# Kernel optimization log

Hardware: AMD Instinct MI355X
Metric: run time of the kernel (lower is better)

## Reference

```python
import jax, jax.numpy as jnp
import numpy as np

HIDDEN = 2048
GAMMA = 0.96875
SCALE_BASE = 512  # XPOS default from torchscale / Jamie-Stirling/RetNet


def _xpos(x, downscale=False):
    # x: [B, L, d]. Faithful port of XPOS with offset=0.
    B, L, d = x.shape
    half = d // 2
    # per-dim scale vector: (arange(0,d,2) + 0.4d) / (1.4d)
    scale_vec = (jnp.arange(0, d, 2, dtype=jnp.float32) + 0.4 * d) / (1.4 * d)  # [half]
    power = jnp.arange(L, dtype=jnp.float32) / SCALE_BASE                        # [L]
    scale = scale_vec[None, :] ** power[:, None]                                 # [L, half]
    # fixed_pos_embedding over `half` frequency dims
    inv_freq = 1.0 / (10000.0 ** (jnp.arange(half, dtype=jnp.float32) / half))   # [half]
    sinusoid = jnp.arange(L, dtype=jnp.float32)[:, None] * inv_freq[None, :]     # [L, half]
    sin, cos = jnp.sin(sinusoid), jnp.cos(sinusoid)
    if downscale:
        scale = 1.0 / scale
    # duplicate_interleave: [L, half] -> [L, d] with each column repeated twice
    sin_s = jnp.repeat(sin * scale, 2, axis=-1)  # [L, d]
    cos_s = jnp.repeat(cos * scale, 2, axis=-1)  # [L, d]
    # rotate_every_two
    x1 = x[..., 0::2]
    x2 = x[..., 1::2]
    rot = jnp.stack((-x2, x1), axis=-1).reshape(x.shape)
    return x * cos_s[None] + rot * sin_s[None]


def _decay_matrix(L):
    n = jnp.arange(L)[:, None]
    m = jnp.arange(L)[None, :]
    mask = n >= m
    # clamp exponent to avoid overflow where masked (torch sets NaN->0)
    D = jnp.where(mask, GAMMA ** jnp.maximum(n - m, 0).astype(jnp.float32), 0.0)
    return D  # [L, L]


def setup_inputs() -> dict:
    key = jax.random.key(0)
    kx, kq, kk, kv = jax.random.split(key, 4)
    B, S, H = 4, 2048, HIDDEN
    X = jax.random.normal(kx, (B, S, H), dtype=jnp.float32)
    W_Q = jax.random.normal(kq, (H, H), dtype=jnp.float32) / H
    W_K = jax.random.normal(kk, (H, H), dtype=jnp.float32) / H
    W_V = jax.random.normal(kv, (H, H), dtype=jnp.float32) / H
    return {"X": X, "W_Q": W_Q, "W_K": W_K, "W_V": W_V}


def reference(X, W_Q, W_K, W_V):
    B, S, H = X.shape
    Q = _xpos(X @ W_Q)                   # [B, S, H]
    K = _xpos(X @ W_K, downscale=True)   # [B, S, H]
    V = X @ W_V                          # [B, S, H]
    D = _decay_matrix(S)                 # [S, S]
    att = jnp.einsum("bnh,bmh->bnm", Q, K) * D[None]  # [B, S, S]
    return att @ V                       # [B, S, H]
```

## Files before the change

kernel.cpp:

```cpp
#include <hip/hip_runtime.h>
#include <math.h>


typedef __attribute__((ext_vector_type(8))) short short8;
typedef __attribute__((ext_vector_type(4))) float f32x4;
typedef __attribute__((ext_vector_type(4))) unsigned short us4;

#define BM 128
#define BN 128
#define BK 64

static __device__ __forceinline__ unsigned short f2bf(float f) {
    unsigned int u = __float_as_uint(f);
    u += 0x7FFFu + ((u >> 16) & 1u);
    return (unsigned short)(u >> 16);
}

static __device__ __forceinline__ void gload16(const unsigned short* g, unsigned short* l) {
    __builtin_amdgcn_global_load_lds(
        (const __attribute__((address_space(1))) unsigned int*)g,
        (__attribute__((address_space(3))) unsigned int*)l, 16, 0, 0);
}

template <int STAGE>
__global__ __launch_bounds__(256)
void gemm_bt(const unsigned short* __restrict__ A,
             const unsigned short* __restrict__ Bt,
             void* __restrict__ Cv,
             unsigned short* __restrict__ Cq,
             unsigned short* __restrict__ Ck,
             unsigned short* __restrict__ Cvt,
             int lda, int ldb, int Kd,
             long long sA, long long sB, long long sC)
{
    constexpr int S = 2048, H = 2048;
    const int rowBase = blockIdx.y * BM;
    const int colBase = blockIdx.x * BN;

    if (STAGE == 3 && blockIdx.x > blockIdx.y) {
        unsigned short* att = (unsigned short*)Cv + (long long)blockIdx.z * sC;
        int r = threadIdx.x >> 1, c = (threadIdx.x & 1) * 64;
        unsigned short* p = att + (size_t)(rowBase + r) * S + colBase + c;
        uint4 z = make_uint4(0, 0, 0, 0);
#pragma unroll
        for (int q = 0; q < 8; ++q) ((uint4*)p)[q] = z;
        return;
    }

    A  += (long long)blockIdx.z * sA;
    Bt += (long long)blockIdx.z * sB;

    __shared__ unsigned short As[BM * BK];
    __shared__ unsigned short Bs[BN * BK];

    const int tid  = threadIdx.x;
    const int wave = tid >> 6;
    const int lane = tid & 63;
    const int wm = (wave & 1) * 64;
    const int wn = (wave >> 1) * 64;

    f32x4 acc[4][4];
#pragma unroll
    for (int i = 0; i < 4; ++i)
#pragma unroll
        for (int j = 0; j < 4; ++j) acc[i][j] = (f32x4){0.f, 0.f, 0.f, 0.f};

    int kmax = Kd;
    if (STAGE == 4) { int km = colBase + BN; kmax = km < Kd ? km : Kd; }

    const int srow = wave * 32 + (lane >> 3);
    const int schunk = ((lane & 7) ^ ((lane >> 3) & 7)) * 8;
    const unsigned short* ga = A  + (size_t)(rowBase + srow) * lda + schunk;
    const unsigned short* gb = Bt + (size_t)(colBase + srow) * ldb + schunk;
    unsigned short* lA = As + wave * 2048;
    unsigned short* lB = Bs + wave * 2048;

#pragma unroll
    for (int q = 0; q < 4; ++q) {
        gload16(ga + (size_t)q * 8 * lda, lA + q * 512);
        gload16(gb + (size_t)q * 8 * ldb, lB + q * 512);
    }

    const int fr = lane & 15;
    const int qd = lane >> 4;
    const int fsw = fr & 7;

    for (int k0 = 0; k0 < kmax; k0 += BK) {
        __syncthreads();
        short8 af0[4], bf0[4], af1[4], bf1[4];
#pragma unroll
        for (int i = 0; i < 4; ++i) {
            int row = wm + i * 16 + fr;
            af0[i] = *(const short8*)&As[row * 64 + ((qd ^ fsw) * 8)];
            af1[i] = *(const short8*)&As[row * 64 + (((4 + qd) ^ fsw) * 8)];
        }
#pragma unroll
        for (int j = 0; j < 4; ++j) {
            int row = wn + j * 16 + fr;
            bf0[j] = *(const short8*)&Bs[row * 64 + ((qd ^ fsw) * 8)];
            bf1[j] = *(const short8*)&Bs[row * 64 + (((4 + qd) ^ fsw) * 8)];
        }
        __syncthreads();
        if (k0 + BK < kmax) {
            const unsigned short* ga2 = ga + k0 + BK;
            const unsigned short* gb2 = gb + k0 + BK;
#pragma unroll
            for (int q = 0; q < 4; ++q) {
                gload16(ga2 + (size_t)q * 8 * lda, lA + q * 512);
                gload16(gb2 + (size_t)q * 8 * ldb, lB + q * 512);
            }
        }
#pragma unroll
        for (int i = 0; i < 4; ++i)
#pragma unroll
            for (int j = 0; j < 4; ++j)
                acc[i][j] = __builtin_amdgcn_mfma_f32_16x16x32_bf16(af0[i], bf0[j], acc[i][j], 0, 0, 0);
#pragma unroll
        for (int i = 0; i < 4; ++i)
#pragma unroll
            for (int j = 0; j < 4; ++j)
                acc[i][j] = __builtin_amdgcn_mfma_f32_16x16x32_bf16(af1[i], bf1[j], acc[i][j], 0, 0, 0);
    }

    if (STAGE == 1) {
        const int mode = colBase >> 11;
        if (mode < 2) {
            unsigned short* Co = (mode == 0) ? Cq : Ck;
            const float psgn = (mode == 1) ? -1.953125e-3f : 1.953125e-3f;
#pragma unroll
            for (int j = 0; j < 4; ++j) {
                int gc = (colBase & 2047) + wn + j * 16 + fr;
                float c0 = (float)(gc & ~1);
                float l2sv = log2f((c0 + 819.2f) * (1.0f / 2867.2f)) * psgn;
                float invf = exp2f(c0 * -0.0064881407f);
                float s1, c1;
                sincosf(invf, &s1, &c1);
#pragma unroll
                for (int i = 0; i < 4; ++i) {
                    int gr0 = rowBase + wm + i * 16 + qd * 4;
                    float fn = (float)(gr0 & (S - 1));
                    float sN, cN;
                    sincosf(fn * invf, &sN, &cN);
#pragma unroll
                    for (int r = 0; r < 4; ++r) {
                        float scale = exp2f(fn * l2sv);
                        float cs = cN * scale, ss = sN * scale;
                        float v = acc[i][j][r];
                        float o = __shfl_xor(v, 1);
                        float res = (gc & 1) ? fmaf(v, cs, o * ss) : fmaf(v, cs, -o * ss);
                        Co[(size_t)(gr0 + r) * H + gc] = f2bf(res);
                        float sn2 = sN * c1 + cN * s1;
                        cN = cN * c1 - sN * s1;
                        sN = sn2;
                        fn += 1.0f;
                    }
                }
            }
        } else {
#pragma unroll
            for (int j = 0; j < 4; ++j) {
                int gh = (colBase & 2047) + wn + j * 16 + fr;
#pragma unroll
                for (int i = 0; i < 4; ++i) {
                    int gm0 = rowBase + wm + i * 16 + qd * 4;
                    us4 p;
#pragma unroll
                    for (int r = 0; r < 4; ++r) p[r] = f2bf(acc[i][j][r]);
                    *(us4*)&Cvt[(size_t)gh * 8192 + gm0] = p;
                }
            }
        }
    } else if (STAGE == 3) {
        unsigned short* att = (unsigned short*)Cv + (long long)blockIdx.z * sC;
#pragma unroll
        for (int j = 0; j < 4; ++j) {
            int m = colBase + wn + j * 16 + fr;
#pragma unroll
            for (int i = 0; i < 4; ++i) {
                int n0 = rowBase + wm + i * 16 + qd * 4;
#pragma unroll
                for (int r = 0; r < 4; ++r) {
                    int d = n0 + r - m;
                    float v = (d >= 0) ? acc[i][j][r] * exp2f((float)d * -0.045803598f) : 0.0f;
                    att[(size_t)(n0 + r) * S + m] = f2bf(v);
                }
            }
        }
    } else {
        float* Co = (float*)Cv + (long long)blockIdx.z * sC;
#pragma unroll
        for (int j = 0; j < 4; ++j) {
            int gn = colBase + wn + j * 16 + fr;
#pragma unroll
            for (int i = 0; i < 4; ++i) {
                int gh0 = rowBase + wm + i * 16 + qd * 4;
                *(f32x4*)&Co[(size_t)gn * H + gh0] = acc[i][j];
            }
        }
    }
}

__global__ __launch_bounds__(256)
void cvt_f32_bf16(const float* __restrict__ x, unsigned short* __restrict__ y) {
    int i = blockIdx.x * 256 + threadIdx.x;
    float4 v = ((const float4*)x)[i];
    us4 o = {f2bf(v.x), f2bf(v.y), f2bf(v.z), f2bf(v.w)};
    ((us4*)y)[i] = o;
}

__global__ __launch_bounds__(256)
void cvt_transpose3(const float* __restrict__ W0, const float* __restrict__ W1,
                    const float* __restrict__ W2, unsigned short* __restrict__ Wt) {
    __shared__ float t[64][65];
    const float* W = (blockIdx.z == 0) ? W0 : (blockIdx.z == 1) ? W1 : W2;
    unsigned short* Wo = Wt + (size_t)blockIdx.z * 4194304;
    int bx = blockIdx.x * 64, by = blockIdx.y * 64;
    int tx = threadIdx.x & 63, ty = threadIdx.x >> 6;
#pragma unroll
    for (int r = 0; r < 64; r += 4)
        t[ty + r][tx] = W[(size_t)(by + ty + r) * 2048 + bx + tx];
    __syncthreads();
#pragma unroll
    for (int r = 0; r < 64; r += 4)
        Wo[(size_t)(bx + ty + r) * 2048 + by + tx] = f2bf(t[tx][ty + r]);
}

extern "C" void kernel_launch(void* const* d_in, const int* in_sizes, int n_in,
                              void* d_out, int out_size, void* d_ws, size_t ws_size,
                              hipStream_t stream) {
    const int S = 2048, H = 2048;
    const long long MH = 16777216;
    const long long HH = 4194304;
    const long long SH = (long long)S * H;
    const long long SS = (long long)S * S;

    const float* X  = (const float*)d_in[0];
    const float* WQ = (const float*)d_in[1];
    const float* WK = (const float*)d_in[2];
    const float* WV = (const float*)d_in[3];
    float* out = (float*)d_out;

    unsigned short* Xb    = (unsigned short*)d_ws;
    unsigned short* WtAll = Xb + MH;
    unsigned short* Qb    = WtAll + 3 * HH;
    unsigned short* Kb    = Qb + MH;
    unsigned short* Vt    = Kb + MH;
    unsigned short* att   = Vt + MH;

    cvt_f32_bf16<<<16384, 256, 0, stream>>>(X, Xb);
    cvt_transpose3<<<dim3(32, 32, 3), 256, 0, stream>>>(WQ, WK, WV, WtAll);

    gemm_bt<1><<<dim3(48, 64), 256, 0, stream>>>(Xb, WtAll, nullptr, Qb, Kb, Vt,
                                                 H, H, H, 0, 0, 0);
    gemm_bt<3><<<dim3(16, 16, 4), 256, 0, stream>>>(Qb, Kb, att, nullptr, nullptr, nullptr,
                                                    H, H, H, SH, SH, SS);
    gemm_bt<4><<<dim3(16, 16, 4), 256, 0, stream>>>(Vt, att, out, nullptr, nullptr, nullptr,
                                                    8192, S, S, S, SS, SH);
}
```

Baseline: 488.0 us.

## Add dedicated 256x128 output GEMM kernel and factor decay exponentials

Replaces the STAGE 4 path of the generic GEMM with a separate gemm_out kernel. It uses 512 threads and a 256x128 tile, loading 256 rows of Vt per block so each loaded att tile is reused across twice as many output rows, and it keeps the causal K-limit. The STAGE 3 epilogue now factors the decay gamma^(n-m) into a per-row exponential times a per-column exponential, which cuts the exp2f calls per element. The XPOS epilogue also replaces its per-row exp2f with a running multiply by the scale step. The larger tile halves the block count to 512 and raises per-block LDS use, which may lower occupancy. The factored exponentials can change rounding slightly.

```diff
diff --git a/kernel.cpp b/kernel.cpp
--- a/kernel.cpp
+++ b/kernel.cpp
@@ -9,6 +9,8 @@
 #define BM 128
 #define BN 128
 #define BK 64
+
+#define LOG2_GAMMA -0.045803598f
 
 static __device__ __forceinline__ unsigned short f2bf(float f) {
     unsigned int u = __float_as_uint(f);
@@ -65,8 +67,7 @@
 #pragma unroll
         for (int j = 0; j < 4; ++j) acc[i][j] = (f32x4){0.f, 0.f, 0.f, 0.f};
 
-    int kmax = Kd;
-    if (STAGE == 4) { int km = colBase + BN; kmax = km < Kd ? km : Kd; }
+    const int kmax = Kd;
 
     const int srow = wave * 32 + (lane >> 3);
     const int schunk = ((lane & 7) ^ ((lane >> 3) & 7)) * 8;
@@ -132,6 +133,7 @@
                 int gc = (colBase & 2047) + wn + j * 16 + fr;
                 float c0 = (float)(gc & ~1);
                 float l2sv = log2f((c0 + 819.2f) * (1.0f / 2867.2f)) * psgn;
+                float sstep = exp2f(l2sv);
                 float invf = exp2f(c0 * -0.0064881407f);
                 float s1, c1;
                 sincosf(invf, &s1, &c1);
@@ -141,9 +143,9 @@
                     float fn = (float)(gr0 & (S - 1));
                     float sN, cN;
                     sincosf(fn * invf, &sN, &cN);
+                    float scale = exp2f(fn * l2sv);
 #pragma unroll
                     for (int r = 0; r < 4; ++r) {
-                        float scale = exp2f(fn * l2sv);
                         float cs = cN * scale, ss = sN * scale;
                         float v = acc[i][j][r];
                         float o = __shfl_xor(v, 1);
@@ -152,7 +154,7 @@
                         float sn2 = sN * c1 + cN * s1;
                         cN = cN * c1 - sN * s1;
                         sN = sn2;
-                        fn += 1.0f;
+                        scale *= sstep;
                     }
                 }
             }
@@ -170,32 +172,122 @@
                 }
             }
         }
-    } else if (STAGE == 3) {
+    } else {
         unsigned short* att = (unsigned short*)Cv + (long long)blockIdx.z * sC;
+        float fj[4];
 #pragma unroll
         for (int j = 0; j < 4; ++j) {
             int m = colBase + wn + j * 16 + fr;
-#pragma unroll
-            for (int i = 0; i < 4; ++i) {
-                int n0 = rowBase + wm + i * 16 + qd * 4;
-#pragma unroll
-                for (int r = 0; r < 4; ++r) {
+            fj[j] = exp2f((float)(colBase - m) * LOG2_GAMMA);
+        }
+#pragma unroll
+        for (int i = 0; i < 4; ++i) {
+            int n0 = rowBase + wm + i * 16 + qd * 4;
+#pragma unroll
+            for (int r = 0; r < 4; ++r) {
+                float ei = exp2f((float)(n0 + r - colBase) * LOG2_GAMMA);
+#pragma unroll
+                for (int j = 0; j < 4; ++j) {
+                    int m = colBase + wn + j * 16 + fr;
                     int d = n0 + r - m;
-                    float v = (d >= 0) ? acc[i][j][r] * exp2f((float)d * -0.045803598f) : 0.0f;
+                    float v = (d >= 0) ? acc[i][j][r] * ei * fj[j] : 0.0f;
                     att[(size_t)(n0 + r) * S + m] = f2bf(v);
                 }
             }
         }
-    } else {
-        float* Co = (float*)Cv + (long long)blockIdx.z * sC;
+    }
+}
+
+__global__ __launch_bounds__(512)
+void gemm_out(const unsigned short* __restrict__ Vt,
+              const unsigned short* __restrict__ attB,
+              float* __restrict__ Outp)
+{
+    constexpr int S = 2048, H = 2048;
+    const int rowBase = blockIdx.y * 256;
+    const int colBase = blockIdx.x * 128;
+    const int z = blockIdx.z;
+
+    const unsigned short* A  = Vt + (size_t)z * 2048;
+    const unsigned short* Bt = attB + (size_t)z * S * S;
+    float* Co = Outp + (size_t)z * S * H;
+
+    __shared__ unsigned short As[256 * BK];
+    __shared__ unsigned short Bs[128 * BK];
+
+    const int tid  = threadIdx.x;
+    const int wave = tid >> 6;
+    const int lane = tid & 63;
+    const int wm = (wave & 3) * 64;
+    const int wn = (wave >> 2) * 64;
+
+    f32x4 acc[4][4];
+#pragma unroll
+    for (int i = 0; i < 4; ++i)
+#pragma unroll
+        for (int j = 0; j < 4; ++j) acc[i][j] = (f32x4){0.f, 0.f, 0.f, 0.f};
+
+    const int kmax = colBase + 128;
+
+    const int subrow = lane >> 3;
+    const int schunk = ((lane & 7) ^ (subrow & 7)) * 8;
+    const unsigned short* ga = A  + (size_t)(rowBase + wave * 32 + subrow) * 8192 + schunk;
+    const unsigned short* gb = Bt + (size_t)(colBase + wave * 16 + subrow) * S + schunk;
+    unsigned short* lA = As + wave * 2048;
+    unsigned short* lB = Bs + wave * 1024;
+
+#pragma unroll
+    for (int q = 0; q < 4; ++q) gload16(ga + (size_t)q * 8 * 8192, lA + q * 512);
+#pragma unroll
+    for (int q = 0; q < 2; ++q) gload16(gb + (size_t)q * 8 * S, lB + q * 512);
+
+    const int fr = lane & 15;
+    const int qd = lane >> 4;
+    const int fsw = fr & 7;
+
+    for (int k0 = 0; k0 < kmax; k0 += BK) {
+        __syncthreads();
+        short8 af0[4], bf0[4], af1[4], bf1[4];
+#pragma unroll
+        for (int i = 0; i < 4; ++i) {
+            int row = wm + i * 16 + fr;
+            af0[i] = *(const short8*)&As[row * 64 + ((qd ^ fsw) * 8)];
+            af1[i] = *(const short8*)&As[row * 64 + (((4 + qd) ^ fsw) * 8)];
+        }
 #pragma unroll
         for (int j = 0; j < 4; ++j) {
-            int gn = colBase + wn + j * 16 + fr;
-#pragma unroll
-            for (int i = 0; i < 4; ++i) {
-                int gh0 = rowBase + wm + i * 16 + qd * 4;
-                *(f32x4*)&Co[(size_t)gn * H + gh0] = acc[i][j];
-            }
+            int row = wn + j * 16 + fr;
+            bf0[j] = *(const short8*)&Bs[row * 64 + ((qd ^ fsw) * 8)];
+            bf1[j] = *(const short8*)&Bs[row * 64 + (((4 + qd) ^ fsw) * 8)];
+        }
+        __syncthreads();
+        if (k0 + BK < kmax) {
+            const unsigned short* ga2 = ga + k0 + BK;
+            const unsigned short* gb2 = gb + k0 + BK;
+#pragma unroll
+            for (int q = 0; q < 4; ++q) gload16(ga2 + (size_t)q * 8 * 8192, lA + q * 512);
+#pragma unroll
+            for (int q = 0; q < 2; ++q) gload16(gb2 + (size_t)q * 8 * S, lB + q * 512);
+        }
+#pragma unroll
+        for (int i = 0; i < 4; ++i)
+#pragma unroll
+            for (int j = 0; j < 4; ++j)
+                acc[i][j] = __builtin_amdgcn_mfma_f32_16x16x32_bf16(af0[i], bf0[j], acc[i][j], 0, 0, 0);
+#pragma unroll
+        for (int i = 0; i < 4; ++i)
+#pragma unroll
+            for (int j = 0; j < 4; ++j)
+                acc[i][j] = __builtin_amdgcn_mfma_f32_16x16x32_bf16(af1[i], bf1[j], acc[i][j], 0, 0, 0);
+    }
+
+#pragma unroll
+    for (int j = 0; j < 4; ++j) {
+        int gn = colBase + wn + j * 16 + fr;
+#pragma unroll
+        for (int i = 0; i < 4; ++i) {
+            int gh0 = rowBase + wm + i * 16 + qd * 4;
+            *(f32x4*)&Co[(size_t)gn * H + gh0] = acc[i][j];
         }
     }
 }
@@ -254,6 +346,5 @@
                                                  H, H, H, 0, 0, 0);
     gemm_bt<3><<<dim3(16, 16, 4), 256, 0, stream>>>(Qb, Kb, att, nullptr, nullptr, nullptr,
                                                     H, H, H, SH, SH, SS);
-    gemm_bt<4><<<dim3(16, 16, 4), 256, 0, stream>>>(Vt, att, out, nullptr, nullptr, nullptr,
-                                                    8192, S, S, S, SS, SH);
-}
+    gemm_out<<<dim3(16, 8, 4), 512, 0, stream>>>(Vt, att, out);
+}
```

Measured after the change: 508.4 us. +4.2%, slower.
